# Kernel optimization log

Measured on AMD Instinct MI355X. Metric: run time of the kernel, lower is better.

## Reference

```python
import jax, jax.numpy as jnp
import numpy as np

B = 8          # graphs (FOVs)
NPG = 16384    # clusters per graph
N = B * NPG
K = 6          # knn k=5+1, loop=True
E = N * K
C0PG = 2048    # superclusters_0 per graph
C0 = B * C0PG
C1PG = 256     # superclusters_1 per graph
C1 = B * C1PG
L = 10         # 4 cluster-level + 3 SC0 + 3 SC1 PointTransformerConv layers
D = 64


def setup_inputs() -> dict:
    key = jax.random.key(0)
    ks = jax.random.split(key, 20)
    s = 0.05  # weight scale for stable attention logits
    x = jax.random.normal(ks[0], (N, D), jnp.float32)
    pos_c = jax.random.uniform(ks[1], (N, 2), jnp.float32)
    dst_c = jnp.repeat(jnp.arange(N, dtype=jnp.int32), K)
    src_c = jax.random.randint(ks[2], (E,), 0, N, jnp.int32)
    src_c = src_c.at[::K].set(jnp.arange(N, dtype=jnp.int32))  # self-loops
    batch = (jnp.arange(N, dtype=jnp.int32) // NPG)
    sc_id0 = (jnp.arange(N, dtype=jnp.int32) % C0PG)   # every SC0 id present per graph
    pos_sc0 = jax.random.uniform(ks[3], (C0, 2), jnp.float32)
    sc_id1 = (jnp.arange(C0, dtype=jnp.int32) % C1PG)
    pos_sc1 = jax.random.uniform(ks[4], (C1, 2), jnp.float32)
    return dict(
        x=x, pos_c=pos_c, src_c=src_c, dst_c=dst_c, batch=batch,
        sc_id0=sc_id0, pos_sc0=pos_sc0, sc_id1=sc_id1, pos_sc1=pos_sc1,
        Wlin=jax.random.normal(ks[5], (L, D, D)) * s,
        Wsrc=jax.random.normal(ks[6], (L, D, D)) * s,
        Wdst=jax.random.normal(ks[7], (L, D, D)) * s,
        pW1=jax.random.normal(ks[8], (L, 2, D)) * s,
        pB1=jnp.zeros((L, D), jnp.float32),
        pW2=jax.random.normal(ks[9], (L, D, D)) * s,
        pB2=jnp.zeros((L, D), jnp.float32),
        aW1=jax.random.normal(ks[10], (L, D, D)) * s,
        aB1=jnp.zeros((L, D), jnp.float32),
        aW2=jax.random.normal(ks[11], (L, D, D)) * s,
        aB2=jnp.zeros((L, D), jnp.float32),
        head_w=jax.random.normal(ks[12], (D, 2)) * s,
        head_b=jnp.zeros((2,), jnp.float32),
    )


def mlp2(x, W1, b1, W2, b2):
    # PyG MLP(plain_last=False): Linear->ReLU twice (eval mode, BN at init = identity)
    h = jax.nn.relu(x @ W1 + b1)
    return jax.nn.relu(h @ W2 + b2)


def ptconv(h, pos, src, dst, n, p, l):
    # PointTransformerConv: delta = pos_nn(pos_i - pos_j);
    # alpha = softmax_i(attn_nn(lin_dst(x)_i - lin_src(x)_j + delta));
    # out_i = max_j alpha * (lin(x)_j + delta)
    xv = h @ p['Wlin'][l]
    a_src = h @ p['Wsrc'][l]
    a_dst = h @ p['Wdst'][l]
    delta = mlp2(pos[dst] - pos[src], p['pW1'][l], p['pB1'][l], p['pW2'][l], p['pB2'][l])
    a = mlp2(a_dst[dst] - a_src[src] + delta, p['aW1'][l], p['aB1'][l], p['aW2'][l], p['aB2'][l])
    m = jax.ops.segment_max(a, dst, num_segments=n)
    e = jnp.exp(a - m[dst])
    ssum = jax.ops.segment_sum(e, dst, num_segments=n)
    alpha = e / ssum[dst]
    return jax.ops.segment_max(alpha * (xv[src] + delta), dst, num_segments=n)


def gen_cluster(ids, batch, nb):
    mx = jax.ops.segment_max(ids, batch, num_segments=nb)
    off = jnp.cumsum(jnp.concatenate([jnp.zeros((1,), ids.dtype), mx + 1]))
    return ids + off[batch].astype(ids.dtype)


def knn_edges(pos, b, npg, k):
    # knn_graph(k, loop=True) per graph: src=neighbor, dst=center
    p = pos.reshape(b, npg, 2)
    sq = jnp.sum(p * p, axis=-1)
    d2 = sq[:, :, None] + sq[:, None, :] - 2.0 * jnp.einsum('bnd,bmd->bnm', p, p)
    idx = jax.lax.top_k(-d2, k)[1]  # [b, npg, k], includes self (d=0)
    src = (idx + (jnp.arange(b) * npg)[:, None, None]).reshape(-1).astype(jnp.int32)
    dst = jnp.repeat(jnp.arange(b * npg, dtype=jnp.int32), k)
    return src, dst


def reference(x, pos_c, src_c, dst_c, batch, sc_id0, pos_sc0, sc_id1, pos_sc1,
              Wlin, Wsrc, Wdst, pW1, pB1, pW2, pB2, aW1, aB1, aW2, aB2,
              head_w, head_b):
    p = dict(Wlin=Wlin, Wsrc=Wsrc, Wdst=Wdst, pW1=pW1, pB1=pB1, pW2=pW2, pB2=pB2,
             aW1=aW1, aB1=aB1, aW2=aW2, aB2=aB2)
    h = x
    for l in range(4):  # cluster_encoder_0..3 on clusters graph
        h = ptconv(h, pos_c, src_c, dst_c, N, p, l)
    # pool clusters -> superclusters_0
    cl0 = gen_cluster(sc_id0, batch, B)
    h0 = jax.ops.segment_max(h, cl0, num_segments=C0)
    batch0 = jax.ops.segment_max(batch, cl0, num_segments=C0)
    src0, dst0 = knn_edges(pos_sc0, B, C0PG, K)
    for l in range(4, 7):
        h0 = ptconv(h0, pos_sc0, src0, dst0, C0, p, l)
    # pool SC0 -> superclusters_1
    cl1 = gen_cluster(sc_id1, batch0, B)
    h1 = jax.ops.segment_max(h0, cl1, num_segments=C1)
    batch1 = jax.ops.segment_max(batch0, cl1, num_segments=C1)
    src1, dst1 = knn_edges(pos_sc1, B, C1PG, K)
    for l in range(7, 10):
        h1 = ptconv(h1, pos_sc1, src1, dst1, C1, p, l)
    g = jax.ops.segment_max(h1, batch1, num_segments=B)  # global_max_pool
    return g @ head_w + head_b
```

## Files before the change

### kernel.cpp

```cpp
#include <hip/hip_runtime.h>
#include <cstdint>

namespace {
constexpr int BG   = 8;
constexpr int NPG  = 16384;
constexpr int NN   = BG * NPG;
constexpr int KK   = 6;
constexpr int C0PG = 2048;
constexpr int C0N  = BG * C0PG;
constexpr int C1PG = 256;
constexpr int C1N  = BG * C1PG;
constexpr int D    = 64;
constexpr int SEG0 = C0PG / 256;
constexpr int VS   = 198;
}

__device__ __forceinline__ unsigned f2u_ord(float v) {
  unsigned u = __float_as_uint(v);
  return (u & 0x80000000u) ? ~u : (u | 0x80000000u);
}

__global__ void k_init_u32(unsigned* __restrict__ p, unsigned v, int n) {
  int i = blockIdx.x * blockDim.x + threadIdx.x;
  if (i < n) p[i] = v;
}

__global__ void k_seg_max_i32(const int* __restrict__ vals, const int* __restrict__ seg,
                              int* __restrict__ out, int n) {
  int i = blockIdx.x * blockDim.x + threadIdx.x;
  if (i < n) atomicMax(&out[seg[i]], vals[i]);
}

template <int NB>
__global__ __launch_bounds__(256) void k_seg_max_small(
    const int* __restrict__ vals, const int* __restrict__ seg,
    int* __restrict__ out, int n) {
  __shared__ int lmx[NB];
  int t = threadIdx.x;
  if (t < NB) lmx[t] = (int)0x80000000;
  __syncthreads();
  for (int i = blockIdx.x * 256 + t; i < n; i += gridDim.x * 256)
    atomicMax(&lmx[seg[i]], vals[i]);
  __syncthreads();
  if (t < NB) atomicMax(&out[t], lmx[t]);
}

__global__ void k_cumsum_off(const int* __restrict__ mx, int* __restrict__ off, int nb) {
  if (threadIdx.x == 0 && blockIdx.x == 0) {
    int a = 0; off[0] = 0;
    for (int b = 0; b < nb; ++b) { a += mx[b] + 1; off[b + 1] = a; }
  }
}

__global__ void k_gen_cl(const int* __restrict__ ids, const int* __restrict__ bt,
                         const int* __restrict__ off, int* __restrict__ cl, int n) {
  int i = blockIdx.x * blockDim.x + threadIdx.x;
  if (i < n) cl[i] = ids[i] + off[bt[i]];
}

__global__ void k_pool_f32(const float* __restrict__ h, const int* __restrict__ cl,
                           unsigned* __restrict__ outu, int total) {
  int i = blockIdx.x * blockDim.x + threadIdx.x;
  if (i < total) atomicMax(&outu[(size_t)cl[i >> 6] * D + (i & 63)], f2u_ord(h[i]));
}

__global__ void k_decode_f32(unsigned* __restrict__ p, int n) {
  int i = blockIdx.x * blockDim.x + threadIdx.x;
  if (i < n) { unsigned u = p[i]; p[i] = (u & 0x80000000u) ? (u ^ 0x80000000u) : ~u; }
}

__global__ __launch_bounds__(256) void k_knn(const float* __restrict__ pos, int npg,
                                             int* __restrict__ srcOut) {
  #pragma clang fp contract(off)
  __shared__ float px[2048], py[2048], sq[2048];
  int t = threadIdx.x;
  int nglob = blockIdx.x * 256 + t;
  int graph = nglob / npg;
  int base = graph * npg;
  for (int i = t; i < npg; i += 256) {
    float xx = pos[2 * (base + i)];
    float yy = pos[2 * (base + i) + 1];
    px[i] = xx; py[i] = yy;
    float a = xx * xx; float b = yy * yy;
    sq[i] = a + b;
  }
  __syncthreads();
  int i = nglob - base;
  float xi = px[i], yi = py[i], sqi = sq[i];
  float bd[KK]; int bi[KK];
  #pragma unroll
  for (int q = 0; q < KK; ++q) { bd[q] = 3.4e38f; bi[q] = 0; }
  for (int j = 0; j < npg; ++j) {
    float t1 = xi * px[j];
    float t2 = yi * py[j];
    float dot = t1 + t2;
    float d2 = (sqi + sq[j]) - 2.0f * dot;
    if (d2 < bd[KK - 1]) {
      bd[KK - 1] = d2; bi[KK - 1] = j;
      #pragma unroll
      for (int q = KK - 1; q > 0; --q) {
        if (bd[q] < bd[q - 1]) {
          float td = bd[q]; bd[q] = bd[q - 1]; bd[q - 1] = td;
          int ti = bi[q]; bi[q] = bi[q - 1]; bi[q - 1] = ti;
        }
      }
    }
  }
  #pragma unroll
  for (int q = 0; q < KK; ++q) srcOut[(size_t)nglob * KK + q] = base + bi[q];
}

__global__ __launch_bounds__(256) void k_knn_part(const float* __restrict__ pos, int npg,
                                                  int nseg,
                                                  float* __restrict__ outD,
                                                  int* __restrict__ outI) {
  #pragma clang fp contract(off)
  __shared__ float cx[256], cy[256], cs[256];
  int t = threadIdx.x;
  int qt = blockIdx.x / nseg;
  int s  = blockIdx.x % nseg;
  int qlo = qt * 256;
  int graph = qlo / npg;
  int base = graph * npg;
  int cbase = base + s * 256;
  {
    float xx = pos[2 * (cbase + t)];
    float yy = pos[2 * (cbase + t) + 1];
    cx[t] = xx; cy[t] = yy;
    float a = xx * xx; float b = yy * yy;
    cs[t] = a + b;
  }
  __syncthreads();
  int q = qlo + t;
  float xi = pos[2 * q], yi = pos[2 * q + 1];
  float qa = xi * xi; float qb = yi * yi;
  float sqi = qa + qb;
  float bd[KK]; int bi[KK];
  #pragma unroll
  for (int u = 0; u < KK; ++u) { bd[u] = 3.4e38f; bi[u] = 0; }
  for (int j = 0; j < 256; ++j) {
    float t1 = xi * cx[j];
    float t2 = yi * cy[j];
    float dot = t1 + t2;
    float d2 = (sqi + cs[j]) - 2.0f * dot;
    if (d2 < bd[KK - 1]) {
      bd[KK - 1] = d2; bi[KK - 1] = cbase + j;
      #pragma unroll
      for (int u = KK - 1; u > 0; --u) {
        if (bd[u] < bd[u - 1]) {
          float td = bd[u]; bd[u] = bd[u - 1]; bd[u - 1] = td;
          int ti = bi[u]; bi[u] = bi[u - 1]; bi[u - 1] = ti;
        }
      }
    }
  }
  size_t ob = (size_t)q * (nseg * KK) + (size_t)s * KK;
  #pragma unroll
  for (int u = 0; u < KK; ++u) { outD[ob + u] = bd[u]; outI[ob + u] = bi[u]; }
}

__global__ void k_knn_merge(const float* __restrict__ inD, const int* __restrict__ inI,
                            int nseg, int* __restrict__ srcOut, int nq) {
  int q = blockIdx.x * blockDim.x + threadIdx.x;
  if (q >= nq) return;
  float bd[KK]; int bi[KK];
  #pragma unroll
  for (int u = 0; u < KK; ++u) { bd[u] = 3.4e38f; bi[u] = 0x7fffffff; }
  size_t ib = (size_t)q * (nseg * KK);
  for (int e = 0; e < nseg * KK; ++e) {
    float d = inD[ib + e]; int ix = inI[ib + e];
    bool lt = (d < bd[KK - 1]) || (d == bd[KK - 1] && ix < bi[KK - 1]);
    if (lt) {
      bd[KK - 1] = d; bi[KK - 1] = ix;
      #pragma unroll
      for (int u = KK - 1; u > 0; --u) {
        bool sw = (bd[u] < bd[u - 1]) || (bd[u] == bd[u - 1] && bi[u] < bi[u - 1]);
        if (sw) {
          float td = bd[u]; bd[u] = bd[u - 1]; bd[u - 1] = td;
          int ti = bi[u]; bi[u] = bi[u - 1]; bi[u - 1] = ti;
        }
      }
    }
  }
  #pragma unroll
  for (int u = 0; u < KK; ++u) srcOut[(size_t)q * KK + u] = bi[u];
}

__global__ __launch_bounds__(256, 2) void k_node_mm(const float* __restrict__ hin,
    const float* __restrict__ Wl, const float* __restrict__ Ws, const float* __restrict__ Wd,
    float* __restrict__ xv, float* __restrict__ as_, float* __restrict__ ad_) {
  __shared__ float wbuf[4096];
  __shared__ float vbuf[32 * 260];
  int t = threadIdx.x;
  size_t nb = (size_t)blockIdx.x * 256;
  int ng = t >> 2, cb = t & 3, c0 = cb * 16;
  const float* Wm[3] = {Wl, Ws, Wd};
  float* Om[3] = {xv, as_, ad_};
  const float4* h4 = (const float4*)hin;
  #pragma unroll
  for (int m = 0; m < 3; ++m) {
    __syncthreads();
    {
      const float4* w4 = (const float4*)Wm[m];
      float4* wb = (float4*)wbuf;
      #pragma unroll
      for (int i = 0; i < 4; ++i) wb[i * 256 + t] = w4[i * 256 + t];
    }
    float acc[64];
    #pragma unroll
    for (int i = 0; i < 64; ++i) acc[i] = 0.0f;
    for (int kh = 0; kh < 2; ++kh) {
      if (kh) __syncthreads();
      #pragma unroll
      for (int r = 0; r < 8; ++r) {
        int flat = r * 256 + t;
        int n = flat >> 3, kq = flat & 7;
        float4 hv = h4[(nb + n) * 16 + kh * 8 + kq];
        vbuf[(kq * 4 + 0) * 260 + n] = hv.x;
        vbuf[(kq * 4 + 1) * 260 + n] = hv.y;
        vbuf[(kq * 4 + 2) * 260 + n] = hv.z;
        vbuf[(kq * 4 + 3) * 260 + n] = hv.w;
      }
      __syncthreads();
      #pragma clang loop unroll_count(2)
      for (int kk = 0; kk < 32; ++kk) {
        int k = kh * 32 + kk;
        float4 v4 = *(const float4*)&vbuf[kk * 260 + 4 * ng];
        float4 wq0 = *(const float4*)&wbuf[k * 64 + c0];
        float4 wq1 = *(const float4*)&wbuf[k * 64 + c0 + 4];
        float4 wq2 = *(const float4*)&wbuf[k * 64 + c0 + 8];
        float4 wq3 = *(const float4*)&wbuf[k * 64 + c0 + 12];
        float vv[4] = {v4.x, v4.y, v4.z, v4.w};
        float wv[16] = {wq0.x, wq0.y, wq0.z, wq0.w, wq1.x, wq1.y, wq1.z, wq1.w,
                        wq2.x, wq2.y, wq2.z, wq2.w, wq3.x, wq3.y, wq3.z, wq3.w};
        #pragma unroll
        for (int ni = 0; ni < 4; ++ni)
          #pragma unroll
          for (int c = 0; c < 16; ++c)
            acc[ni * 16 + c] = fmaf(vv[ni], wv[c], acc[ni * 16 + c]);
      }
    }
    float* O = Om[m];
    #pragma unroll
    for (int ni = 0; ni < 4; ++ni)
      #pragma unroll
      for (int q = 0; q < 4; ++q)
        *(float4*)(O + (nb + 4 * ng + ni) * 64 + c0 + 4 * q) =
            make_float4(acc[ni * 16 + 4 * q], acc[ni * 16 + 4 * q + 1],
                        acc[ni * 16 + 4 * q + 2], acc[ni * 16 + 4 * q + 3]);
  }
}

__global__ __launch_bounds__(256, 2) void k_edge_fused(
    const float* __restrict__ pos, const int* __restrict__ srcA,
    const float* __restrict__ as_, const float* __restrict__ ad_,
    const float* __restrict__ xv,
    const float* __restrict__ pW1, const float* __restrict__ pB1,
    const float* __restrict__ pW2, const float* __restrict__ pB2,
    const float* __restrict__ aW1, const float* __restrict__ aB1,
    const float* __restrict__ aW2, const float* __restrict__ aB2,
    float* __restrict__ hout) {
  __shared__ float wbuf[4096];
  __shared__ float vbuf[64 * VS];
  __shared__ float sbuf[192];
  __shared__ float pdxs[192], pdys[192];
  __shared__ int   srcb[192];
  int t = threadIdx.x;
  int nb = blockIdx.x * 32;
  int ng = t >> 3;
  int cb = t & 7;
  int c0 = cb * 8;
  int node = nb + ng;

  if (t < 192) {
    int s = srcA[(size_t)nb * KK + t];
    srcb[t] = s;
    int dn = nb + t / KK;
    float2 pd = *(const float2*)(pos + 2 * (size_t)dn);
    float2 ps = *(const float2*)(pos + 2 * (size_t)s);
    pdxs[t] = pd.x - ps.x;
    pdys[t] = pd.y - ps.y;
    sbuf[t] = (t < 128) ? pW1[t] : pB1[t - 128];
  }
  {
    const float4* w4 = (const float4*)pW2;
    float4* wb = (float4*)wbuf;
    #pragma unroll
    for (int i = 0; i < 4; ++i) wb[i * 256 + t] = w4[i * 256 + t];
  }
  __syncthreads();

  if (t < 192) {
    float px = pdxs[t], py = pdys[t];
    #pragma clang loop unroll_count(4)
    for (int k = 0; k < 64; ++k) {
      float p0 = px * sbuf[k];
      float p1 = py * sbuf[64 + k];
      float ph = fmaxf((p0 + p1) + sbuf[128 + k], 0.0f);
      vbuf[k * VS + t] = ph;
    }
  }
  __syncthreads();

  float d[48];
  {
    float4 b0 = *(const float4*)(pB2 + c0);
    float4 b1 = *(const float4*)(pB2 + c0 + 4);
    #pragma unroll
    for (int j = 0; j < 6; ++j) {
      d[j * 8 + 0] = b0.x; d[j * 8 + 1] = b0.y; d[j * 8 + 2] = b0.z; d[j * 8 + 3] = b0.w;
      d[j * 8 + 4] = b1.x; d[j * 8 + 5] = b1.y; d[j * 8 + 6] = b1.z; d[j * 8 + 7] = b1.w;
    }
  }
  #pragma clang loop unroll_count(2)
  for (int k = 0; k < 64; ++k) {
    float2 v01 = *(const float2*)&vbuf[k * VS + 6 * ng];
    float2 v23 = *(const float2*)&vbuf[k * VS + 6 * ng + 2];
    float2 v45 = *(const float2*)&vbuf[k * VS + 6 * ng + 4];
    float4 w0 = *(const float4*)&wbuf[k * 64 + c0];
    float4 w1 = *(const float4*)&wbuf[k * 64 + c0 + 4];
    float vv[6] = {v01.x, v01.y, v23.x, v23.y, v45.x, v45.y};
    float wv[8] = {w0.x, w0.y, w0.z, w0.w, w1.x, w1.y, w1.z, w1.w};
    #pragma unroll
    for (int j = 0; j < 6; ++j)
      #pragma unroll
      for (int c = 0; c < 8; ++c)
        d[j * 8 + c] = fmaf(vv[j], wv[c], d[j * 8 + c]);
  }
  #pragma unroll
  for (int i = 0; i < 48; ++i) d[i] = fmaxf(d[i], 0.0f);

  __syncthreads();
  {
    const float4* w4 = (const float4*)aW1;
    float4* wb = (float4*)wbuf;
    #pragma unroll
    for (int i = 0; i < 4; ++i) wb[i * 256 + t] = w4[i * 256 + t];
  }
  {
    float4 a0 = *(const float4*)(ad_ + (size_t)node * 64 + c0);
    float4 a1 = *(const float4*)(ad_ + (size_t)node * 64 + c0 + 4);
    #pragma unroll
    for (int j = 0; j < 6; ++j) {
      int s = srcb[6 * ng + j];
      float4 s0 = *(const float4*)(as_ + (size_t)s * 64 + c0);
      float4 s1 = *(const float4*)(as_ + (size_t)s * 64 + c0 + 4);
      float vj[8];
      vj[0] = (a0.x - s0.x) + d[j * 8 + 0];
      vj[1] = (a0.y - s0.y) + d[j * 8 + 1];
      vj[2] = (a0.z - s0.z) + d[j * 8 + 2];
      vj[3] = (a0.w - s0.w) + d[j * 8 + 3];
      vj[4] = (a1.x - s1.x) + d[j * 8 + 4];
      vj[5] = (a1.y - s1.y) + d[j * 8 + 5];
      vj[6] = (a1.z - s1.z) + d[j * 8 + 6];
      vj[7] = (a1.w - s1.w) + d[j * 8 + 7];
      #pragma unroll
      for (int cj = 0; cj < 8; ++cj) vbuf[(c0 + cj) * VS + 6 * ng + j] = vj[cj];
    }
  }
  __syncthreads();
  float r[48];
  {
    float4 b0 = *(const float4*)(aB1 + c0);
    float4 b1 = *(const float4*)(aB1 + c0 + 4);
    #pragma unroll
    for (int j = 0; j < 6; ++j) {
      r[j * 8 + 0] = b0.x; r[j * 8 + 1] = b0.y; r[j * 8 + 2] = b0.z; r[j * 8 + 3] = b0.w;
      r[j * 8 + 4] = b1.x; r[j * 8 + 5] = b1.y; r[j * 8 + 6] = b1.z; r[j * 8 + 7] = b1.w;
    }
  }
  #pragma clang loop unroll_count(2)
  for (int k = 0; k < 64; ++k) {
    float2 v01 = *(const float2*)&vbuf[k * VS + 6 * ng];
    float2 v23 = *(const float2*)&vbuf[k * VS + 6 * ng + 2];
    float2 v45 = *(const float2*)&vbuf[k * VS + 6 * ng + 4];
    float4 w0 = *(const float4*)&wbuf[k * 64 + c0];
    float4 w1 = *(const float4*)&wbuf[k * 64 + c0 + 4];
    float vv[6] = {v01.x, v01.y, v23.x, v23.y, v45.x, v45.y};
    float wv[8] = {w0.x, w0.y, w0.z, w0.w, w1.x, w1.y, w1.z, w1.w};
    #pragma unroll
    for (int j = 0; j < 6; ++j)
      #pragma unroll
      for (int c = 0; c < 8; ++c)
        r[j * 8 + c] = fmaf(vv[j], wv[c], r[j * 8 + c]);
  }
  #pragma unroll
  for (int i = 0; i < 48; ++i) r[i] = fmaxf(r[i], 0.0f);

  __syncthreads();
  {
    const float4* w4 = (const float4*)aW2;
    float4* wb = (float4*)wbuf;
    #pragma unroll
    for (int i = 0; i < 4; ++i) wb[i * 256 + t] = w4[i * 256 + t];
  }
  #pragma unroll
  for (int j = 0; j < 6; ++j)
    #pragma unroll
    for (int cj = 0; cj < 8; ++cj) vbuf[(c0 + cj) * VS + 6 * ng + j] = r[j * 8 + cj];
  __syncthreads();
  float a[48];
  {
    float4 b0 = *(const float4*)(aB2 + c0);
    float4 b1 = *(const float4*)(aB2 + c0 + 4);
    #pragma unroll
    for (int j = 0; j < 6; ++j) {
      a[j * 8 + 0] = b0.x; a[j * 8 + 1] = b0.y; a[j * 8 + 2] = b0.z; a[j * 8 + 3] = b0.w;
      a[j * 8 + 4] = b1.x; a[j * 8 + 5] = b1.y; a[j * 8 + 6] = b1.z; a[j * 8 + 7] = b1.w;
    }
  }
  #pragma clang loop unroll_count(2)
  for (int k = 0; k < 64; ++k) {
    float2 v01 = *(const float2*)&vbuf[k * VS + 6 * ng];
    float2 v23 = *(const float2*)&vbuf[k * VS + 6 * ng + 2];
    float2 v45 = *(const float2*)&vbuf[k * VS + 6 * ng + 4];
    float4 w0 = *(const float4*)&wbuf[k * 64 + c0];
    float4 w1 = *(const float4*)&wbuf[k * 64 + c0 + 4];
    float vv[6] = {v01.x, v01.y, v23.x, v23.y, v45.x, v45.y};
    float wv[8] = {w0.x, w0.y, w0.z, w0.w, w1.x, w1.y, w1.z, w1.w};
    #pragma unroll
    for (int j = 0; j < 6; ++j)
      #pragma unroll
      for (int c = 0; c < 8; ++c)
        a[j * 8 + c] = fmaf(vv[j], wv[c], a[j * 8 + c]);
  }
  #pragma unroll
  for (int i = 0; i < 48; ++i) a[i] = fmaxf(a[i], 0.0f);

  float m8[8], ss[8], out[8];
  #pragma unroll
  for (int c = 0; c < 8; ++c) m8[c] = a[c];
  #pragma unroll
  for (int j = 1; j < 6; ++j)
    #pragma unroll
    for (int c = 0; c < 8; ++c) m8[c] = fmaxf(m8[c], a[j * 8 + c]);
  #pragma unroll
  for (int c = 0; c < 8; ++c) ss[c] = 0.0f;
  #pragma unroll
  for (int j = 0; j < 6; ++j)
    #pragma unroll
    for (int c = 0; c < 8; ++c) ss[c] += expf(a[j * 8 + c] - m8[c]);
  #pragma unroll
  for (int j = 0; j < 6; ++j) {
    int s = srcb[6 * ng + j];
    float4 x0 = *(const float4*)(xv + (size_t)s * 64 + c0);
    float4 x1 = *(const float4*)(xv + (size_t)s * 64 + c0 + 4);
    float xa[8] = {x0.x, x0.y, x0.z, x0.w, x1.x, x1.y, x1.z, x1.w};
    #pragma unroll
    for (int c = 0; c < 8; ++c) {
      float ej = expf(a[j * 8 + c] - m8[c]);
      float alpha = ej / ss[c];
      float val = alpha * (xa[c] + d[j * 8 + c]);
      out[c] = (j == 0) ? val : fmaxf(out[c], val);
    }
  }
  *(float4*)(hout + (size_t)node * 64 + c0) = make_float4(out[0], out[1], out[2], out[3]);
  *(float4*)(hout + (size_t)node * 64 + c0 + 4) = make_float4(out[4], out[5], out[6], out[7]);
}

__global__ void k_head(const float* __restrict__ g, const float* __restrict__ hw,
                       const float* __restrict__ hb, float* __restrict__ out) {
  int t = threadIdx.x;
  if (t >= BG * 2) return;
  int b = t >> 1, o = t & 1;
  float acc = 0.0f;
  for (int k = 0; k < D; ++k) acc = fmaf(g[b * D + k], hw[k * 2 + o], acc);
  out[b * 2 + o] = acc + hb[o];
}

extern "C" void kernel_launch(void* const* d_in, const int* in_sizes, int n_in,
                              void* d_out, int out_size, void* d_ws, size_t ws_size,
                              hipStream_t stream) {
  (void)in_sizes; (void)n_in; (void)out_size; (void)ws_size;
  const float* x      = (const float*)d_in[0];
  const float* pos_c  = (const float*)d_in[1];
  const int*   src_c  = (const int*)d_in[2];
  const int*   batch  = (const int*)d_in[4];
  const int*   sc_id0 = (const int*)d_in[5];
  const float* pos_s0 = (const float*)d_in[6];
  const int*   sc_id1 = (const int*)d_in[7];
  const float* pos_s1 = (const float*)d_in[8];
  const float* Wlin = (const float*)d_in[9];
  const float* Wsrc = (const float*)d_in[10];
  const float* Wdst = (const float*)d_in[11];
  const float* pW1  = (const float*)d_in[12];
  const float* pB1  = (const float*)d_in[13];
  const float* pW2  = (const float*)d_in[14];
  const float* pB2  = (const float*)d_in[15];
  const float* aW1  = (const float*)d_in[16];
  const float* aB1  = (const float*)d_in[17];
  const float* aW2  = (const float*)d_in[18];
  const float* aB2  = (const float*)d_in[19];
  const float* hw   = (const float*)d_in[20];
  const float* hb   = (const float*)d_in[21];
  float* outp = (float*)d_out;

  char* ws = (char*)d_ws;
  size_t off = 0;
  auto alloc = [&](size_t bytes) -> void* {
    void* p = ws + off; off = (off + bytes + 255) & ~(size_t)255; return p;
  };
  float* h   = (float*)alloc((size_t)NN * D * 4);
  float* xv  = (float*)alloc((size_t)NN * D * 4);
  float* as_ = (float*)alloc((size_t)NN * D * 4);
  float* ad_ = (float*)alloc((size_t)NN * D * 4);
  float* h0  = (float*)alloc((size_t)C0N * D * 4);
  float* h1  = (float*)alloc((size_t)C1N * D * 4);
  float* g   = (float*)alloc((size_t)BG * D * 4);
  int* cl0   = (int*)alloc((size_t)NN * 4);
  int* cl1   = (int*)alloc((size_t)C0N * 4);
  int* b0    = (int*)alloc((size_t)C0N * 4);
  int* b1    = (int*)alloc((size_t)C1N * 4);
  int* src0  = (int*)alloc((size_t)C0N * KK * 4);
  int* src1  = (int*)alloc((size_t)C1N * KK * 4);
  float* kd  = (float*)alloc((size_t)C0N * SEG0 * KK * 4);
  int*   ki  = (int*)alloc((size_t)C0N * SEG0 * KK * 4);
  int* mx    = (int*)alloc(256);
  int* offb  = (int*)alloc(256);

  auto ptconv = [&](int n, const float* pos, const int* srcA,
                    const float* hin, float* hout, int l) {
    k_node_mm<<<n / 256, 256, 0, stream>>>(hin,
        Wlin + (size_t)l * 4096, Wsrc + (size_t)l * 4096, Wdst + (size_t)l * 4096,
        xv, as_, ad_);
    k_edge_fused<<<n / 32, 256, 0, stream>>>(pos, srcA, as_, ad_, xv,
        pW1 + (size_t)l * 128, pB1 + (size_t)l * 64,
        pW2 + (size_t)l * 4096, pB2 + (size_t)l * 64,
        aW1 + (size_t)l * 4096, aB1 + (size_t)l * 64,
        aW2 + (size_t)l * 4096, aB2 + (size_t)l * 64,
        hout);
  };

  k_init_u32<<<1, 64, 0, stream>>>((unsigned*)mx, 0x80000000u, BG);
  k_seg_max_small<BG><<<64, 256, 0, stream>>>(sc_id0, batch, mx, NN);
  k_cumsum_off<<<1, 1, 0, stream>>>(mx, offb, BG);
  k_gen_cl<<<NN / 256, 256, 0, stream>>>(sc_id0, batch, offb, cl0, NN);
  k_init_u32<<<(C0N + 255) / 256, 256, 0, stream>>>((unsigned*)b0, 0x80000000u, C0N);
  k_seg_max_i32<<<NN / 256, 256, 0, stream>>>(batch, cl0, b0, NN);
  k_knn_part<<<(C0N / 256) * SEG0, 256, 0, stream>>>(pos_s0, C0PG, SEG0, kd, ki);
  k_knn_merge<<<C0N / 256, 256, 0, stream>>>(kd, ki, SEG0, src0, C0N);
  k_init_u32<<<1, 64, 0, stream>>>((unsigned*)mx, 0x80000000u, BG);
  k_seg_max_small<BG><<<64, 256, 0, stream>>>(sc_id1, b0, mx, C0N);
  k_cumsum_off<<<1, 1, 0, stream>>>(mx, offb, BG);
  k_gen_cl<<<C0N / 256, 256, 0, stream>>>(sc_id1, b0, offb, cl1, C0N);
  k_init_u32<<<(C1N + 255) / 256, 256, 0, stream>>>((unsigned*)b1, 0x80000000u, C1N);
  k_seg_max_i32<<<C0N / 256, 256, 0, stream>>>(b0, cl1, b1, C0N);
  k_knn<<<C1N / 256, 256, 0, stream>>>(pos_s1, C1PG, src1);

  ptconv(NN, pos_c, src_c, x, h, 0);
  for (int l = 1; l < 4; ++l) ptconv(NN, pos_c, src_c, h, h, l);
  k_init_u32<<<C0N * D / 256, 256, 0, stream>>>((unsigned*)h0, 0x007fffffu, C0N * D);
  k_pool_f32<<<NN * D / 256, 256, 0, stream>>>(h, cl0, (unsigned*)h0, NN * D);
  k_decode_f32<<<C0N * D / 256, 256, 0, stream>>>((unsigned*)h0, C0N * D);
  for (int l = 4; l < 7; ++l) ptconv(C0N, pos_s0, src0, h0, h0, l);
  k_init_u32<<<C1N * D / 256, 256, 0, stream>>>((unsigned*)h1, 0x007fffffu, C1N * D);
  k_pool_f32<<<C0N * D / 256, 256, 0, stream>>>(h0, cl1, (unsigned*)h1, C0N * D);
  k_decode_f32<<<C1N * D / 256, 256, 0, stream>>>((unsigned*)h1, C1N * D);
  for (int l = 7; l < 10; ++l) ptconv(C1N, pos_s1, src1, h1, h1, l);
  k_init_u32<<<(BG * D + 255) / 256, 256, 0, stream>>>((unsigned*)g, 0x007fffffu, BG * D);
  k_pool_f32<<<C1N * D / 256, 256, 0, stream>>>(h1, b1, (unsigned*)g, C1N * D);
  k_decode_f32<<<(BG * D + 255) / 256, 256, 0, stream>>>((unsigned*)g, BG * D);
  k_head<<<1, 64, 0, stream>>>(g, hw, hb, outp);
}
```

Baseline: 2.114 ms.

## Halve shared memory via K-split tiles to raise occupancy in node and edge kernels

Both the node matmul and the fused edge kernel now stage weights and activations in two 32-row halves of the reduction dimension instead of full 64-row tiles. This cuts LDS per block roughly in half, so launch bounds can rise to 4 blocks per CU. The node kernel now processes 128 nodes per block and accumulates all three projections together, which reuses the staged input tile. The edge kernel remaps channel ownership to two separated 4-wide groups so the transposed vbuf writes can use float2 stores. The cost is more barriers and weight reloads per block, and register pressure under the tighter launch bound.

```diff
diff --git a/kernel.cpp b/kernel.cpp
--- a/kernel.cpp
+++ b/kernel.cpp
@@ -13,6 +13,7 @@
 constexpr int D    = 64;
 constexpr int SEG0 = C0PG / 256;
 constexpr int VS   = 198;
+constexpr int NMS  = 132;
 }
 
 __device__ __forceinline__ unsigned f2u_ord(float v) {
@@ -186,72 +187,74 @@
   for (int u = 0; u < KK; ++u) srcOut[(size_t)q * KK + u] = bi[u];
 }
 
-__global__ __launch_bounds__(256, 2) void k_node_mm(const float* __restrict__ hin,
+__global__ __launch_bounds__(256, 4) void k_node_mm(const float* __restrict__ hin,
     const float* __restrict__ Wl, const float* __restrict__ Ws, const float* __restrict__ Wd,
     float* __restrict__ xv, float* __restrict__ as_, float* __restrict__ ad_) {
-  __shared__ float wbuf[4096];
-  __shared__ float vbuf[32 * 260];
+  __shared__ float wbuf[2048];
+  __shared__ float vbuf[32 * NMS];
   int t = threadIdx.x;
-  size_t nb = (size_t)blockIdx.x * 256;
-  int ng = t >> 2, cb = t & 3, c0 = cb * 16;
+  size_t nb = (size_t)blockIdx.x * 128;
+  int ng = t >> 3, cb = t & 7, c0 = cb * 8;
   const float* Wm[3] = {Wl, Ws, Wd};
   float* Om[3] = {xv, as_, ad_};
   const float4* h4 = (const float4*)hin;
-  #pragma unroll
-  for (int m = 0; m < 3; ++m) {
-    __syncthreads();
-    {
-      const float4* w4 = (const float4*)Wm[m];
-      float4* wb = (float4*)wbuf;
-      #pragma unroll
-      for (int i = 0; i < 4; ++i) wb[i * 256 + t] = w4[i * 256 + t];
-    }
-    float acc[64];
-    #pragma unroll
-    for (int i = 0; i < 64; ++i) acc[i] = 0.0f;
-    for (int kh = 0; kh < 2; ++kh) {
-      if (kh) __syncthreads();
-      #pragma unroll
-      for (int r = 0; r < 8; ++r) {
-        int flat = r * 256 + t;
-        int n = flat >> 3, kq = flat & 7;
-        float4 hv = h4[(nb + n) * 16 + kh * 8 + kq];
-        vbuf[(kq * 4 + 0) * 260 + n] = hv.x;
-        vbuf[(kq * 4 + 1) * 260 + n] = hv.y;
-        vbuf[(kq * 4 + 2) * 260 + n] = hv.z;
-        vbuf[(kq * 4 + 3) * 260 + n] = hv.w;
+  float acc[3][32];
+  #pragma unroll
+  for (int m = 0; m < 3; ++m)
+    #pragma unroll
+    for (int i = 0; i < 32; ++i) acc[m][i] = 0.0f;
+  for (int kh = 0; kh < 2; ++kh) {
+    #pragma unroll
+    for (int r = 0; r < 4; ++r) {
+      int flat = r * 256 + t;
+      int n = flat >> 3, kq = flat & 7;
+      float4 hv = h4[(nb + n) * 16 + kh * 8 + kq];
+      vbuf[(kq * 4 + 0) * NMS + n] = hv.x;
+      vbuf[(kq * 4 + 1) * NMS + n] = hv.y;
+      vbuf[(kq * 4 + 2) * NMS + n] = hv.z;
+      vbuf[(kq * 4 + 3) * NMS + n] = hv.w;
+    }
+    #pragma unroll
+    for (int m = 0; m < 3; ++m) {
+      {
+        const float4* w4 = (const float4*)Wm[m] + kh * 512;
+        float4* wb = (float4*)wbuf;
+        wb[t] = w4[t];
+        wb[256 + t] = w4[256 + t];
       }
       __syncthreads();
       #pragma clang loop unroll_count(2)
       for (int kk = 0; kk < 32; ++kk) {
-        int k = kh * 32 + kk;
-        float4 v4 = *(const float4*)&vbuf[kk * 260 + 4 * ng];
-        float4 wq0 = *(const float4*)&wbuf[k * 64 + c0];
-        float4 wq1 = *(const float4*)&wbuf[k * 64 + c0 + 4];
-        float4 wq2 = *(const float4*)&wbuf[k * 64 + c0 + 8];
-        float4 wq3 = *(const float4*)&wbuf[k * 64 + c0 + 12];
+        float4 v4 = *(const float4*)&vbuf[kk * NMS + 4 * ng];
+        float4 w0 = *(const float4*)&wbuf[kk * 64 + c0];
+        float4 w1 = *(const float4*)&wbuf[kk * 64 + c0 + 4];
         float vv[4] = {v4.x, v4.y, v4.z, v4.w};
-        float wv[16] = {wq0.x, wq0.y, wq0.z, wq0.w, wq1.x, wq1.y, wq1.z, wq1.w,
-                        wq2.x, wq2.y, wq2.z, wq2.w, wq3.x, wq3.y, wq3.z, wq3.w};
+        float wv[8] = {w0.x, w0.y, w0.z, w0.w, w1.x, w1.y, w1.z, w1.w};
         #pragma unroll
         for (int ni = 0; ni < 4; ++ni)
           #pragma unroll
-          for (int c = 0; c < 16; ++c)
-            acc[ni * 16 + c] = fmaf(vv[ni], wv[c], acc[ni * 16 + c]);
-      }
-    }
+          for (int c = 0; c < 8; ++c)
+            acc[m][ni * 8 + c] = fmaf(vv[ni], wv[c], acc[m][ni * 8 + c]);
+      }
+      __syncthreads();
+    }
+  }
+  #pragma unroll
+  for (int m = 0; m < 3; ++m) {
     float* O = Om[m];
     #pragma unroll
-    for (int ni = 0; ni < 4; ++ni)
-      #pragma unroll
-      for (int q = 0; q < 4; ++q)
-        *(float4*)(O + (nb + 4 * ng + ni) * 64 + c0 + 4 * q) =
-            make_float4(acc[ni * 16 + 4 * q], acc[ni * 16 + 4 * q + 1],
-                        acc[ni * 16 + 4 * q + 2], acc[ni * 16 + 4 * q + 3]);
-  }
-}
-
-__global__ __launch_bounds__(256, 2) void k_edge_fused(
+    for (int ni = 0; ni < 4; ++ni) {
+      *(float4*)(O + (nb + 4 * ng + ni) * 64 + c0) =
+          make_float4(acc[m][ni * 8 + 0], acc[m][ni * 8 + 1],
+                      acc[m][ni * 8 + 2], acc[m][ni * 8 + 3]);
+      *(float4*)(O + (nb + 4 * ng + ni) * 64 + c0 + 4) =
+          make_float4(acc[m][ni * 8 + 4], acc[m][ni * 8 + 5],
+                      acc[m][ni * 8 + 6], acc[m][ni * 8 + 7]);
+    }
+  }
+}
+
+__global__ __launch_bounds__(256, 4) void k_edge_fused(
     const float* __restrict__ pos, const int* __restrict__ srcA,
     const float* __restrict__ as_, const float* __restrict__ ad_,
     const float* __restrict__ xv,
@@ -260,8 +263,8 @@
     const float* __restrict__ aW1, const float* __restrict__ aB1,
     const float* __restrict__ aW2, const float* __restrict__ aB2,
     float* __restrict__ hout) {
-  __shared__ float wbuf[4096];
-  __shared__ float vbuf[64 * VS];
+  __shared__ float wbuf[2048];
+  __shared__ float vbuf[32 * VS];
   __shared__ float sbuf[192];
   __shared__ float pdxs[192], pdys[192];
   __shared__ int   srcb[192];
@@ -269,7 +272,8 @@
   int nb = blockIdx.x * 32;
   int ng = t >> 3;
   int cb = t & 7;
-  int c0 = cb * 8;
+  int cl = 4 * cb;
+  int ch = 32 + 4 * cb;
   int node = nb + ng;
 
   if (t < 192) {
@@ -282,147 +286,158 @@
     pdys[t] = pd.y - ps.y;
     sbuf[t] = (t < 128) ? pW1[t] : pB1[t - 128];
   }
-  {
-    const float4* w4 = (const float4*)pW2;
-    float4* wb = (float4*)wbuf;
-    #pragma unroll
-    for (int i = 0; i < 4; ++i) wb[i * 256 + t] = w4[i * 256 + t];
-  }
-  __syncthreads();
-
-  if (t < 192) {
-    float px = pdxs[t], py = pdys[t];
-    #pragma clang loop unroll_count(4)
-    for (int k = 0; k < 64; ++k) {
-      float p0 = px * sbuf[k];
-      float p1 = py * sbuf[64 + k];
-      float ph = fmaxf((p0 + p1) + sbuf[128 + k], 0.0f);
-      vbuf[k * VS + t] = ph;
-    }
-  }
   __syncthreads();
 
   float d[48];
   {
-    float4 b0 = *(const float4*)(pB2 + c0);
-    float4 b1 = *(const float4*)(pB2 + c0 + 4);
+    float4 b0 = *(const float4*)(pB2 + cl);
+    float4 b1 = *(const float4*)(pB2 + ch);
     #pragma unroll
     for (int j = 0; j < 6; ++j) {
       d[j * 8 + 0] = b0.x; d[j * 8 + 1] = b0.y; d[j * 8 + 2] = b0.z; d[j * 8 + 3] = b0.w;
       d[j * 8 + 4] = b1.x; d[j * 8 + 5] = b1.y; d[j * 8 + 6] = b1.z; d[j * 8 + 7] = b1.w;
     }
   }
-  #pragma clang loop unroll_count(2)
-  for (int k = 0; k < 64; ++k) {
-    float2 v01 = *(const float2*)&vbuf[k * VS + 6 * ng];
-    float2 v23 = *(const float2*)&vbuf[k * VS + 6 * ng + 2];
-    float2 v45 = *(const float2*)&vbuf[k * VS + 6 * ng + 4];
-    float4 w0 = *(const float4*)&wbuf[k * 64 + c0];
-    float4 w1 = *(const float4*)&wbuf[k * 64 + c0 + 4];
-    float vv[6] = {v01.x, v01.y, v23.x, v23.y, v45.x, v45.y};
-    float wv[8] = {w0.x, w0.y, w0.z, w0.w, w1.x, w1.y, w1.z, w1.w};
-    #pragma unroll
-    for (int j = 0; j < 6; ++j)
-      #pragma unroll
-      for (int c = 0; c < 8; ++c)
-        d[j * 8 + c] = fmaf(vv[j], wv[c], d[j * 8 + c]);
+  #pragma unroll
+  for (int h = 0; h < 2; ++h) {
+    {
+      const float4* w4 = (const float4*)pW2 + h * 512;
+      float4* wb = (float4*)wbuf;
+      wb[t] = w4[t];
+      wb[256 + t] = w4[256 + t];
+    }
+    if (t < 192) {
+      float px = pdxs[t], py = pdys[t];
+      #pragma clang loop unroll_count(4)
+      for (int kk = 0; kk < 32; ++kk) {
+        int k = h * 32 + kk;
+        float p0 = px * sbuf[k];
+        float p1 = py * sbuf[64 + k];
+        float ph = fmaxf((p0 + p1) + sbuf[128 + k], 0.0f);
+        vbuf[kk * VS + t] = ph;
+      }
+    }
+    __syncthreads();
+    #pragma clang loop unroll_count(2)
+    for (int kk = 0; kk < 32; ++kk) {
+      float2 v01 = *(const float2*)&vbuf[kk * VS + 6 * ng];
+      float2 v23 = *(const float2*)&vbuf[kk * VS + 6 * ng + 2];
+      float2 v45 = *(const float2*)&vbuf[kk * VS + 6 * ng + 4];
+      float4 w0 = *(const float4*)&wbuf[kk * 64 + cl];
+      float4 w1 = *(const float4*)&wbuf[kk * 64 + ch];
+      float vv[6] = {v01.x, v01.y, v23.x, v23.y, v45.x, v45.y};
+      float wv[8] = {w0.x, w0.y, w0.z, w0.w, w1.x, w1.y, w1.z, w1.w};
+      #pragma unroll
+      for (int j = 0; j < 6; ++j)
+        #pragma unroll
+        for (int c = 0; c < 8; ++c)
+          d[j * 8 + c] = fmaf(vv[j], wv[c], d[j * 8 + c]);
+    }
+    __syncthreads();
   }
   #pragma unroll
   for (int i = 0; i < 48; ++i) d[i] = fmaxf(d[i], 0.0f);
 
-  __syncthreads();
-  {
-    const float4* w4 = (const float4*)aW1;
-    float4* wb = (float4*)wbuf;
-    #pragma unroll
-    for (int i = 0; i < 4; ++i) wb[i * 256 + t] = w4[i * 256 + t];
-  }
-  {
-    float4 a0 = *(const float4*)(ad_ + (size_t)node * 64 + c0);
-    float4 a1 = *(const float4*)(ad_ + (size_t)node * 64 + c0 + 4);
-    #pragma unroll
-    for (int j = 0; j < 6; ++j) {
-      int s = srcb[6 * ng + j];
-      float4 s0 = *(const float4*)(as_ + (size_t)s * 64 + c0);
-      float4 s1 = *(const float4*)(as_ + (size_t)s * 64 + c0 + 4);
-      float vj[8];
-      vj[0] = (a0.x - s0.x) + d[j * 8 + 0];
-      vj[1] = (a0.y - s0.y) + d[j * 8 + 1];
-      vj[2] = (a0.z - s0.z) + d[j * 8 + 2];
-      vj[3] = (a0.w - s0.w) + d[j * 8 + 3];
-      vj[4] = (a1.x - s1.x) + d[j * 8 + 4];
-      vj[5] = (a1.y - s1.y) + d[j * 8 + 5];
-      vj[6] = (a1.z - s1.z) + d[j * 8 + 6];
-      vj[7] = (a1.w - s1.w) + d[j * 8 + 7];
-      #pragma unroll
-      for (int cj = 0; cj < 8; ++cj) vbuf[(c0 + cj) * VS + 6 * ng + j] = vj[cj];
-    }
-  }
-  __syncthreads();
   float r[48];
   {
-    float4 b0 = *(const float4*)(aB1 + c0);
-    float4 b1 = *(const float4*)(aB1 + c0 + 4);
+    float4 b0 = *(const float4*)(aB1 + cl);
+    float4 b1 = *(const float4*)(aB1 + ch);
     #pragma unroll
     for (int j = 0; j < 6; ++j) {
       r[j * 8 + 0] = b0.x; r[j * 8 + 1] = b0.y; r[j * 8 + 2] = b0.z; r[j * 8 + 3] = b0.w;
       r[j * 8 + 4] = b1.x; r[j * 8 + 5] = b1.y; r[j * 8 + 6] = b1.z; r[j * 8 + 7] = b1.w;
     }
   }
-  #pragma clang loop unroll_count(2)
-  for (int k = 0; k < 64; ++k) {
-    float2 v01 = *(const float2*)&vbuf[k * VS + 6 * ng];
-    float2 v23 = *(const float2*)&vbuf[k * VS + 6 * ng + 2];
-    float2 v45 = *(const float2*)&vbuf[k * VS + 6 * ng + 4];
-    float4 w0 = *(const float4*)&wbuf[k * 64 + c0];
-    float4 w1 = *(const float4*)&wbuf[k * 64 + c0 + 4];
-    float vv[6] = {v01.x, v01.y, v23.x, v23.y, v45.x, v45.y};
-    float wv[8] = {w0.x, w0.y, w0.z, w0.w, w1.x, w1.y, w1.z, w1.w};
-    #pragma unroll
-    for (int j = 0; j < 6; ++j)
-      #pragma unroll
-      for (int c = 0; c < 8; ++c)
-        r[j * 8 + c] = fmaf(vv[j], wv[c], r[j * 8 + c]);
+  #pragma unroll
+  for (int h = 0; h < 2; ++h) {
+    {
+      const float4* w4 = (const float4*)aW1 + h * 512;
+      float4* wb = (float4*)wbuf;
+      wb[t] = w4[t];
+      wb[256 + t] = w4[256 + t];
+    }
+    {
+      int cbase = h ? ch : cl;
+      float4 av = *(const float4*)(ad_ + (size_t)node * 64 + cbase);
+      float vtmp[6][4];
+      #pragma unroll
+      for (int j = 0; j < 6; ++j) {
+        int s = srcb[6 * ng + j];
+        float4 sv = *(const float4*)(as_ + (size_t)s * 64 + cbase);
+        vtmp[j][0] = (av.x - sv.x) + d[j * 8 + 4 * h + 0];
+        vtmp[j][1] = (av.y - sv.y) + d[j * 8 + 4 * h + 1];
+        vtmp[j][2] = (av.z - sv.z) + d[j * 8 + 4 * h + 2];
+        vtmp[j][3] = (av.w - sv.w) + d[j * 8 + 4 * h + 3];
+      }
+      #pragma unroll
+      for (int cj = 0; cj < 4; ++cj)
+        #pragma unroll
+        for (int jp = 0; jp < 3; ++jp)
+          *(float2*)&vbuf[(4 * cb + cj) * VS + 6 * ng + 2 * jp] =
+              make_float2(vtmp[2 * jp][cj], vtmp[2 * jp + 1][cj]);
+    }
+    __syncthreads();
+    #pragma clang loop unroll_count(2)
+    for (int kk = 0; kk < 32; ++kk) {
+      float2 v01 = *(const float2*)&vbuf[kk * VS + 6 * ng];
+      float2 v23 = *(const float2*)&vbuf[kk * VS + 6 * ng + 2];
+      float2 v45 = *(const float2*)&vbuf[kk * VS + 6 * ng + 4];
+      float4 w0 = *(const float4*)&wbuf[kk * 64 + cl];
+      float4 w1 = *(const float4*)&wbuf[kk * 64 + ch];
+      float vv[6] = {v01.x, v01.y, v23.x, v23.y, v45.x, v45.y};
+      float wv[8] = {w0.x, w0.y, w0.z, w0.w, w1.x, w1.y, w1.z, w1.w};
+      #pragma unroll
+      for (int j = 0; j < 6; ++j)
+        #pragma unroll
+        for (int c = 0; c < 8; ++c)
+          r[j * 8 + c] = fmaf(vv[j], wv[c], r[j * 8 + c]);
+    }
+    __syncthreads();
   }
   #pragma unroll
   for (int i = 0; i < 48; ++i) r[i] = fmaxf(r[i], 0.0f);
 
-  __syncthreads();
-  {
-    const float4* w4 = (const float4*)aW2;
-    float4* wb = (float4*)wbuf;
-    #pragma unroll
-    for (int i = 0; i < 4; ++i) wb[i * 256 + t] = w4[i * 256 + t];
-  }
-  #pragma unroll
-  for (int j = 0; j < 6; ++j)
-    #pragma unroll
-    for (int cj = 0; cj < 8; ++cj) vbuf[(c0 + cj) * VS + 6 * ng + j] = r[j * 8 + cj];
-  __syncthreads();
   float a[48];
   {
-    float4 b0 = *(const float4*)(aB2 + c0);
-    float4 b1 = *(const float4*)(aB2 + c0 + 4);
+    float4 b0 = *(const float4*)(aB2 + cl);
+    float4 b1 = *(const float4*)(aB2 + ch);
     #pragma unroll
     for (int j = 0; j < 6; ++j) {
       a[j * 8 + 0] = b0.x; a[j * 8 + 1] = b0.y; a[j * 8 + 2] = b0.z; a[j * 8 + 3] = b0.w;
       a[j * 8 + 4] = b1.x; a[j * 8 + 5] = b1.y; a[j * 8 + 6] = b1.z; a[j * 8 + 7] = b1.w;
     }
   }
-  #pragma clang loop unroll_count(2)
-  for (int k = 0; k < 64; ++k) {
-    float2 v01 = *(const float2*)&vbuf[k * VS + 6 * ng];
-    float2 v23 = *(const float2*)&vbuf[k * VS + 6 * ng + 2];
-    float2 v45 = *(const float2*)&vbuf[k * VS + 6 * ng + 4];
-    float4 w0 = *(const float4*)&wbuf[k * 64 + c0];
-    float4 w1 = *(const float4*)&wbuf[k * 64 + c0 + 4];
-    float vv[6] = {v01.x, v01.y, v23.x, v23.y, v45.x, v45.y};
-    float wv[8] = {w0.x, w0.y, w0.z, w0.w, w1.x, w1.y, w1.z, w1.w};
-    #pragma unroll
-    for (int j = 0; j < 6; ++j)
-      #pragma unroll
-      for (int c = 0; c < 8; ++c)
-        a[j * 8 + c] = fmaf(vv[j], wv[c], a[j * 8 + c]);
+  #pragma unroll
+  for (int h = 0; h < 2; ++h) {
+    {
+      const float4* w4 = (const float4*)aW2 + h * 512;
+      float4* wb = (float4*)wbuf;
+      wb[t] = w4[t];
+      wb[256 + t] = w4[256 + t];
+    }
+    #pragma unroll
+    for (int cj = 0; cj < 4; ++cj)
+      #pragma unroll
+      for (int jp = 0; jp < 3; ++jp)
+        *(float2*)&vbuf[(4 * cb + cj) * VS + 6 * ng + 2 * jp] =
+            make_float2(r[(2 * jp) * 8 + 4 * h + cj], r[(2 * jp + 1) * 8 + 4 * h + cj]);
+    __syncthreads();
+    #pragma clang loop unroll_count(2)
+    for (int kk = 0; kk < 32; ++kk) {
+      float2 v01 = *(const float2*)&vbuf[kk * VS + 6 * ng];
+      float2 v23 = *(const float2*)&vbuf[kk * VS + 6 * ng + 2];
+      float2 v45 = *(const float2*)&vbuf[kk * VS + 6 * ng + 4];
+      float4 w0 = *(const float4*)&wbuf[kk * 64 + cl];
+      float4 w1 = *(const float4*)&wbuf[kk * 64 + ch];
+      float vv[6] = {v01.x, v01.y, v23.x, v23.y, v45.x, v45.y};
+      float wv[8] = {w0.x, w0.y, w0.z, w0.w, w1.x, w1.y, w1.z, w1.w};
+      #pragma unroll
+      for (int j = 0; j < 6; ++j)
+        #pragma unroll
+        for (int c = 0; c < 8; ++c)
+          a[j * 8 + c] = fmaf(vv[j], wv[c], a[j * 8 + c]);
+    }
+    __syncthreads();
   }
   #pragma unroll
   for (int i = 0; i < 48; ++i) a[i] = fmaxf(a[i], 0.0f);
@@ -443,8 +458,8 @@
   #pragma unroll
   for (int j = 0; j < 6; ++j) {
     int s = srcb[6 * ng + j];
-    float4 x0 = *(const float4*)(xv + (size_t)s * 64 + c0);
-    float4 x1 = *(const float4*)(xv + (size_t)s * 64 + c0 + 4);
+    float4 x0 = *(const float4*)(xv + (size_t)s * 64 + cl);
+    float4 x1 = *(const float4*)(xv + (size_t)s * 64 + ch);
     float xa[8] = {x0.x, x0.y, x0.z, x0.w, x1.x, x1.y, x1.z, x1.w};
     #pragma unroll
     for (int c = 0; c < 8; ++c) {
@@ -454,8 +469,8 @@
       out[c] = (j == 0) ? val : fmaxf(out[c], val);
     }
   }
-  *(float4*)(hout + (size_t)node * 64 + c0) = make_float4(out[0], out[1], out[2], out[3]);
-  *(float4*)(hout + (size_t)node * 64 + c0 + 4) = make_float4(out[4], out[5], out[6], out[7]);
+  *(float4*)(hout + (size_t)node * 64 + cl) = make_float4(out[0], out[1], out[2], out[3]);
+  *(float4*)(hout + (size_t)node * 64 + ch) = make_float4(out[4], out[5], out[6], out[7]);
 }
 
 __global__ void k_head(const float* __restrict__ g, const float* __restrict__ hw,
@@ -520,7 +535,7 @@
 
   auto ptconv = [&](int n, const float* pos, const int* srcA,
                     const float* hin, float* hout, int l) {
-    k_node_mm<<<n / 256, 256, 0, stream>>>(hin,
+    k_node_mm<<<n / 128, 256, 0, stream>>>(hin,
         Wlin + (size_t)l * 4096, Wsrc + (size_t)l * 4096, Wdst + (size_t)l * 4096,
         xv, as_, ad_);
     k_edge_fused<<<n / 32, 256, 0, stream>>>(pos, srcA, as_, ad_, xv,
```

New measurement: 1.908 ms. 1.11x faster.
